# Performance work log

Hardware: AMD Instinct MI355X
Metric: run time of the kernel (lower is better)

## Reference

```python
import jax, jax.numpy as jnp
import numpy as np

D_MODEL = 1024
N_HEADS = 16
HEAD_DIM = D_MODEL // N_HEADS


def setup_inputs() -> dict:
    key = jax.random.key(0)
    k1, k2, k3, k4, k5 = jax.random.split(key, 5)
    s = 1.0 / np.sqrt(D_MODEL)
    return {
        "x": jax.random.normal(k1, (2, 2048, D_MODEL), dtype=jnp.float32),
        "w_qkv": jax.random.normal(k2, (D_MODEL, 3 * D_MODEL), dtype=jnp.float32) * s,
        "b_qkv": jax.random.normal(k3, (3 * D_MODEL,), dtype=jnp.float32) * 0.02,
        "w_proj": jax.random.normal(k4, (D_MODEL, D_MODEL), dtype=jnp.float32) * s,
        "b_proj": jax.random.normal(k5, (D_MODEL,), dtype=jnp.float32) * 0.02,
    }


def reference(x, w_qkv, b_qkv, w_proj, b_proj):
    B, S, D = x.shape
    H, Hd = N_HEADS, HEAD_DIM
    qkv = x @ w_qkv + b_qkv                       # [B,S,3D]
    q, k, v = jnp.split(qkv, 3, axis=-1)
    # split heads -> [B,H,S,Hd]
    q = q.reshape(B, S, H, Hd).transpose(0, 2, 1, 3)
    k = k.reshape(B, S, H, Hd).transpose(0, 2, 1, 3)
    v = v.reshape(B, S, H, Hd).transpose(0, 2, 1, 3)
    scale = 1.0 / jnp.sqrt(jnp.asarray(Hd, dtype=x.dtype))
    scores = jnp.einsum("bhqd,bhkd->bhqk", q, k) * scale  # [B,H,S,S]
    causal = jnp.tril(jnp.ones((S, S), dtype=bool))
    scores = jnp.where(causal, scores, jnp.asarray(-jnp.inf, dtype=scores.dtype))
    attn = jax.nn.softmax(scores, axis=-1)
    out = jnp.einsum("bhqk,bhkd->bhqd", attn, v)  # [B,H,S,Hd]
    out = out.transpose(0, 2, 1, 3).reshape(B, S, D)
    return out @ w_proj + b_proj
```

## Files before the change

kernel.cpp:

```cpp
#include <hip/hip_runtime.h>


typedef float f32x4 __attribute__((ext_vector_type(4)));
typedef float f32x16 __attribute__((ext_vector_type(16)));
typedef short bf16x8 __attribute__((ext_vector_type(8)));

#if __has_builtin(__builtin_amdgcn_exp2f)
#define EXP2(x) __builtin_amdgcn_exp2f(x)
#else
#define EXP2(x) exp2f(x)
#endif

__device__ __forceinline__ unsigned short f2bf(float f) {
  union { float f; unsigned u; } v; v.f = f;
  unsigned u = v.u + 0x7fffu + ((v.u >> 16) & 1u);
  return (unsigned short)(u >> 16);
}

__device__ __forceinline__ void async_load16(const void* g, void* lds) {
  __builtin_amdgcn_global_load_lds(
      (const __attribute__((address_space(1))) void*)g,
      (__attribute__((address_space(3))) void*)lds, 16, 0, 0);
}

__global__ void f32_to_bf16_kernel(const float* __restrict__ in,
                                   unsigned short* __restrict__ out, int n) {
  int i = (blockIdx.x * 256 + threadIdx.x) * 4;
  if (i < n) {
    float4 f = *(const float4*)(in + i);
    ushort4 o;
    o.x = f2bf(f.x); o.y = f2bf(f.y); o.z = f2bf(f.z); o.w = f2bf(f.w);
    *(ushort4*)(out + i) = o;
  }
}

__global__ void transpose_f32_bf16_kernel(const float* __restrict__ in,
                                          unsigned short* __restrict__ out,
                                          int K, int N) {
  __shared__ float tile[32][33];
  int n0 = blockIdx.x * 32, k0 = blockIdx.y * 32;
  int tx = threadIdx.x, ty = threadIdx.y;
#pragma unroll
  for (int i = ty; i < 32; i += 8)
    tile[i][tx] = in[(size_t)(k0 + i) * N + (n0 + tx)];
  __syncthreads();
#pragma unroll
  for (int i = ty; i < 32; i += 8)
    out[(size_t)(n0 + i) * K + (k0 + tx)] = f2bf(tile[tx][i]);
}

template <int MI, int NI>
__device__ __forceinline__ void gemm_mainloop(
    const unsigned short* __restrict__ A,
    const unsigned short* __restrict__ BT,
    int K, int mBlk, int nBlk,
    unsigned short* As, unsigned short* Bs,
    f32x4 (&acc)[MI][NI], int lane, int wave)
{
  const int l16 = lane & 15, quad = lane >> 4;
  const int mW = (wave >> 1) * MI * 16;
  const int nW = (wave & 1) * NI * 16;
  constexpr int AROWS = 2 * MI * 16;
  constexpr int BROWS = 2 * NI * 16;
  constexpr int AINST = AROWS / 64;
  constexpr int BINST = BROWS / 64;
  const int rl = lane >> 2;
  const int cl = (lane & 3) * 8;

  for (int k0 = 0; k0 < K; k0 += 32) {
    __syncthreads();
#pragma unroll
    for (int t = 0; t < AINST; ++t) {
      const int rbase = wave * (AROWS / 4) + t * 16;
      async_load16(A + (size_t)(mBlk + rbase + rl) * K + k0 + cl, &As[rbase * 32]);
    }
#pragma unroll
    for (int t = 0; t < BINST; ++t) {
      const int rbase = wave * (BROWS / 4) + t * 16;
      async_load16(BT + (size_t)(nBlk + rbase + rl) * K + k0 + cl, &Bs[rbase * 32]);
    }
    __syncthreads();

    bf16x8 af[MI], bf[NI];
#pragma unroll
    for (int i = 0; i < MI; ++i)
      af[i] = *(const bf16x8*)&As[(mW + i * 16 + l16) * 32 + quad * 8];
#pragma unroll
    for (int j = 0; j < NI; ++j)
      bf[j] = *(const bf16x8*)&Bs[(nW + j * 16 + l16) * 32 + quad * 8];
#pragma unroll
    for (int i = 0; i < MI; ++i)
#pragma unroll
      for (int j = 0; j < NI; ++j)
        acc[i][j] = __builtin_amdgcn_mfma_f32_16x16x32_bf16(af[i], bf[j], acc[i][j], 0, 0, 0);
  }
}

__global__ __launch_bounds__(512, 2) void qkv_gemm_kernel(
    const unsigned short* __restrict__ A,
    const unsigned short* __restrict__ WT,
    const float* __restrict__ bias,
    unsigned short* __restrict__ QKV)
{
  __shared__ __align__(16) unsigned short Al[2][2][256][32];
  __shared__ __align__(16) unsigned short Bl[2][2][256][32];
  const int lane = threadIdx.x & 63;
  const int wave = threadIdx.x >> 6;
  const int l16 = lane & 15, quad = lane >> 4;
  const int wm = wave >> 2, wn = wave & 3;

  const int bid = blockIdx.x;
  const int swz = (bid & 7) * 24 + (bid >> 3);
  const int bx = swz & 15, by = swz >> 4;
  const int mBlk = bx * 256, nBlk = by * 256;

  const int srow = wave * 32 + (lane >> 2);
  const int scol = lane & 3;

  auto stage = [&](const unsigned short* __restrict__ G, int gRow0,
                   unsigned short (*L)[32], int kOff) {
#pragma unroll
    for (int i = 0; i < 2; ++i) {
      const int row = srow + i * 16;
      const int c = scol ^ ((row >> 1) & 3);
      async_load16(G + (size_t)(gRow0 + row) * 1024 + kOff + c * 8,
                   &L[wave * 32 + i * 16][0]);
    }
  };

  auto rdA = [&](int buf, int kc, int mi) -> bf16x8 {
    const int r = wm * 128 + mi * 16 + l16;
    return *(const bf16x8*)&Al[buf][kc][r][(quad ^ ((r >> 1) & 3)) * 8];
  };
  auto rdB = [&](int buf, int kc, int n) -> bf16x8 {
    const int r = wn * 64 + n * 16 + l16;
    return *(const bf16x8*)&Bl[buf][kc][r][(quad ^ ((r >> 1) & 3)) * 8];
  };

  f32x4 acc[8][4];
  const f32x4 z4 = {0.f, 0.f, 0.f, 0.f};
#pragma unroll
  for (int i = 0; i < 8; ++i)
#pragma unroll
    for (int j = 0; j < 4; ++j) acc[i][j] = z4;

  stage(A, mBlk, Al[0][0], 0);
  stage(WT, nBlk, Bl[0][0], 0);
  stage(A, mBlk, Al[0][1], 32);
  stage(WT, nBlk, Bl[0][1], 32);
  asm volatile("s_waitcnt vmcnt(4)\n\ts_barrier" ::: "memory");

  for (int t = 0; t < 16; ++t) {
    const int cur = t & 1, nxt = cur ^ 1;
    const int tn = (t + 1 < 16) ? t + 1 : 15;
    const int kO = tn * 64;
    bf16x8 bf0[4], bf1[4], af[4];

    stage(A, mBlk, Al[nxt][0], kO);
#pragma unroll
    for (int n = 0; n < 4; ++n) bf0[n] = rdB(cur, 0, n);
#pragma unroll
    for (int mi = 0; mi < 4; ++mi) af[mi] = rdA(cur, 0, mi);
    __builtin_amdgcn_s_setprio(1);
#pragma unroll
    for (int mi = 0; mi < 4; ++mi)
#pragma unroll
      for (int n = 0; n < 4; ++n)
        acc[mi][n] = __builtin_amdgcn_mfma_f32_16x16x32_bf16(af[mi], bf0[n], acc[mi][n], 0, 0, 0);
    __builtin_amdgcn_s_setprio(0);
    asm volatile("s_waitcnt vmcnt(2)\n\ts_barrier" ::: "memory");

    stage(WT, nBlk, Bl[nxt][0], kO);
#pragma unroll
    for (int n = 0; n < 4; ++n) bf1[n] = rdB(cur, 1, n);
#pragma unroll
    for (int mi = 0; mi < 4; ++mi) af[mi] = rdA(cur, 1, mi);
    __builtin_amdgcn_s_setprio(1);
#pragma unroll
    for (int mi = 0; mi < 4; ++mi)
#pragma unroll
      for (int n = 0; n < 4; ++n)
        acc[mi][n] = __builtin_amdgcn_mfma_f32_16x16x32_bf16(af[mi], bf1[n], acc[mi][n], 0, 0, 0);
    __builtin_amdgcn_s_setprio(0);
    asm volatile("s_barrier" ::: "memory");

    stage(A, mBlk, Al[nxt][1], kO + 32);
#pragma unroll
    for (int mi = 0; mi < 4; ++mi) af[mi] = rdA(cur, 0, mi + 4);
    __builtin_amdgcn_s_setprio(1);
#pragma unroll
    for (int mi = 0; mi < 4; ++mi)
#pragma unroll
      for (int n = 0; n < 4; ++n)
        acc[mi + 4][n] = __builtin_amdgcn_mfma_f32_16x16x32_bf16(af[mi], bf0[n], acc[mi + 4][n], 0, 0, 0);
    __builtin_amdgcn_s_setprio(0);
    asm volatile("s_barrier" ::: "memory");

    stage(WT, nBlk, Bl[nxt][1], kO + 32);
#pragma unroll
    for (int mi = 0; mi < 4; ++mi) af[mi] = rdA(cur, 1, mi + 4);
    __builtin_amdgcn_s_setprio(1);
#pragma unroll
    for (int mi = 0; mi < 4; ++mi)
#pragma unroll
      for (int n = 0; n < 4; ++n)
        acc[mi + 4][n] = __builtin_amdgcn_mfma_f32_16x16x32_bf16(af[mi], bf1[n], acc[mi + 4][n], 0, 0, 0);
    __builtin_amdgcn_s_setprio(0);
    asm volatile("s_waitcnt vmcnt(4)\n\ts_barrier" ::: "memory");
  }
  asm volatile("s_waitcnt vmcnt(0)" ::: "memory");

  const int m0 = mBlk + wm * 128;
  const int n0 = nBlk + wn * 64;
  const int whichW = n0 >> 10;
  const int bb = m0 >> 11;
  const int sBase = (m0 & 2047);
  const size_t planeE = (size_t)2 * 16 * 2048 * 64;

  if (whichW == 2) {
    unsigned short* Vb = QKV + 2 * planeE;
#pragma unroll
    for (int j = 0; j < 4; ++j) {
      const int rem = (n0 & 1023) + j * 16 + l16;
      const int hh = rem >> 6, hd = rem & 63;
      const float bv = bias[n0 + j * 16 + l16];
      unsigned short* col = Vb + (((size_t)bb * 16 + hh) * 64 + hd) * 2048;
#pragma unroll
      for (int i = 0; i < 8; ++i) {
        unsigned short pk[4];
#pragma unroll
        for (int r = 0; r < 4; ++r) pk[r] = f2bf(acc[i][j][r] + bv);
        *(ushort4*)&col[sBase + i * 16 + quad * 4] = *(ushort4*)pk;
      }
    }
  } else {
    const float scale = (whichW == 0) ? 0.18033688011112042f : 1.0f;
#pragma unroll
    for (int j = 0; j < 4; ++j) {
      const int n = n0 + j * 16 + l16;
      const float bv = bias[n];
      const int rem = n & 1023;
      const int hh = rem >> 6, hd = rem & 63;
      unsigned short* pl = QKV + (size_t)whichW * planeE +
                           (((size_t)bb * 16 + hh) * 2048) * 64 + hd;
#pragma unroll
      for (int r = 0; r < 4; ++r) {
        const int s = sBase + (quad * 4 + r);
#pragma unroll
        for (int i = 0; i < 8; ++i)
          pl[(size_t)(s + i * 16) * 64] = f2bf((acc[i][j][r] + bv) * scale);
      }
    }
  }
}

__global__ __launch_bounds__(256, 2) void attn_kernel(
    const unsigned short* __restrict__ QKV,
    unsigned short* __restrict__ AO)
{
  __shared__ __align__(16) unsigned short Ks[3 * 64 * 64];
  __shared__ __align__(16) unsigned short Vs[3 * 64 * 64];
  const int lane = threadIdx.x & 63;
  const int wave = threadIdx.x >> 6;
  const int l31 = lane & 31;
  const int hi  = lane >> 5;

  const int lin  = blockIdx.x;
  const int xcd  = lin & 7;
  const int slot = lin >> 3;
  const int col  = xcd * 4 + (slot >> 4);
  const int b = col >> 4, h = col & 15;
  const int qg = (slot < 32) ? (slot & 15) : (15 - (slot & 15));
  const int qw = qg * 128 + wave * 32;

  const size_t planeE = (size_t)2 * 16 * 2048 * 64;
  const size_t bhS = ((size_t)b * 16 + h) * (size_t)(2048 * 64);
  const unsigned short* Q   = QKV + bhS;
  const unsigned short* Kg  = QKV + planeE + bhS;
  const unsigned short* VTg = QKV + 2 * planeE + bhS;

  bf16x8 qf_[4];
#pragma unroll
  for (int t = 0; t < 4; ++t)
    qf_[t] = *(const bf16x8*)(Q + (size_t)(qw + l31) * 64 + t * 16 + hi * 8);

  bf16x8 onesf;
#pragma unroll
  for (int i = 0; i < 8; ++i) onesf[i] = (short)0x3F80;

  f32x16 O[2], Osum;
#pragma unroll
  for (int r = 0; r < 16; ++r) { O[0][r] = 0.f; O[1][r] = 0.f; Osum[r] = 0.f; }

  const int tbase = (wave & 1) * 4;
  const bool doV = wave >= 2;

  auto stage = [&](int tileIdx, int bufIdx) {
    const int kt = tileIdx * 64;
    unsigned short* Kb = Ks + bufIdx * 4096;
    unsigned short* Vb = Vs + bufIdx * 4096;
#pragma unroll
    for (int i = 0; i < 4; ++i) {
      const int t = tbase + i;
      const int s = t * 64 + lane;
      const int row = s >> 3;
      const int c = (s & 7) ^ (row & 7);
      if (doV)
        async_load16(VTg + (size_t)row * 2048 + kt + c * 8, Vb + t * 512);
      else
        async_load16(Kg + (size_t)(kt + row) * 64 + c * 8, Kb + t * 512);
    }
  };

  const int nt = qg * 2 + 2;
  stage(0, 0);
  stage(1, 1);
  for (int ti = 0; ti < nt; ++ti) {
    asm volatile("s_waitcnt vmcnt(4)\n\ts_barrier" ::: "memory");
    const int tn = (ti + 2 < nt) ? ti + 2 : nt - 1;
    stage(tn, (ti + 2) % 3);
    const int kt = ti * 64;
    const unsigned short* Kb = Ks + (ti % 3) * 4096;
    const unsigned short* Vb = Vs + (ti % 3) * 4096;

    if (kt <= qw + 31) {
      const bool dmask = (kt + 63 > qw);
#pragma unroll
      for (int kg = 0; kg < 2; ++kg) {
        const int krow = kg * 32 + l31;
        const int ks7 = krow & 7;
        bf16x8 ka[4];
#pragma unroll
        for (int t = 0; t < 4; ++t)
          ka[t] = *(const bf16x8*)&Kb[(krow * 8 + ((t * 2 + hi) ^ ks7)) * 8];

        f32x16 sc;
#pragma unroll
        for (int r = 0; r < 16; ++r) sc[r] = 0.f;
        __builtin_amdgcn_s_setprio(1);
#pragma unroll
        for (int t = 0; t < 4; ++t)
          sc = __builtin_amdgcn_mfma_f32_32x32x16_bf16(ka[t], qf_[t], sc, 0, 0, 0);
        __builtin_amdgcn_s_setprio(0);

        float p[16];
#pragma unroll
        for (int r = 0; r < 16; ++r) {
          float v = sc[r];
          if (dmask) {
            const int key = kt + kg * 32 + (r & 3) + 8 * (r >> 2) + 4 * hi;
            if (key > qw + l31) v = -INFINITY;
          }
          p[r] = EXP2(v);
        }
        unsigned c8[8];
#pragma unroll
        for (int i = 0; i < 8; ++i)
          asm("v_cvt_pk_bf16_f32 %0, %1, %2"
              : "=v"(c8[i]) : "v"(p[2 * i]), "v"(p[2 * i + 1]));

#pragma unroll
        for (int half = 0; half < 2; ++half) {
          unsigned a0 = c8[4 * half + 0], a1 = c8[4 * half + 1];
          unsigned a2 = c8[4 * half + 2], a3 = c8[4 * half + 3];
          asm("v_permlane32_swap_b32 %0, %1" : "+v"(a0), "+v"(a2));
          asm("v_permlane32_swap_b32 %0, %1" : "+v"(a1), "+v"(a3));
          union { unsigned u[4]; bf16x8 v; } pa;
          pa.u[0] = a0; pa.u[1] = a1; pa.u[2] = a2; pa.u[3] = a3;
          const int kc = kg * 2 + half;

          __builtin_amdgcn_s_setprio(1);
          Osum = __builtin_amdgcn_mfma_f32_32x32x16_bf16(pa.v, onesf, Osum, 0, 0, 0);
#pragma unroll
          for (int g = 0; g < 2; ++g) {
            const int vrow = g * 32 + l31;
            bf16x8 vb = *(const bf16x8*)&Vb[(vrow * 8 + ((kc * 2 + hi) ^ (vrow & 7))) * 8];
            O[g] = __builtin_amdgcn_mfma_f32_32x32x16_bf16(pa.v, vb, O[g], 0, 0, 0);
          }
          __builtin_amdgcn_s_setprio(0);
        }
      }
    }
  }

  unsigned short* base = AO + ((size_t)b * 2048 + qw) * 1024 + h * 64 + l31;
#pragma unroll
  for (int r = 0; r < 16; ++r) {
    const float inv = 1.0f / Osum[r];
    const int row = (r & 3) + 8 * (r >> 2) + 4 * hi;
#pragma unroll
    for (int g = 0; g < 2; ++g)
      base[(size_t)row * 1024 + g * 32] = f2bf(O[g][r] * inv);
  }
}

__global__ __launch_bounds__(256) void proj_gemm_kernel(
    const unsigned short* __restrict__ A,
    const unsigned short* __restrict__ WT,
    const float* __restrict__ bias,
    float* __restrict__ out)
{
  __shared__ unsigned short As[64 * 32];
  __shared__ unsigned short Bs[128 * 32];
  const int lane = threadIdx.x & 63;
  const int wave = threadIdx.x >> 6;
  const int l16 = lane & 15, quad = lane >> 4;

  f32x4 acc[2][4];
  const f32x4 z4 = {0.f, 0.f, 0.f, 0.f};
#pragma unroll
  for (int i = 0; i < 2; ++i)
#pragma unroll
    for (int j = 0; j < 4; ++j) acc[i][j] = z4;

  gemm_mainloop<2, 4>(A, WT, 1024, blockIdx.x * 64, blockIdx.y * 128,
                      As, Bs, acc, lane, wave);

  const int m0 = blockIdx.x * 64 + (wave >> 1) * 32;
  const int n0 = blockIdx.y * 128 + (wave & 1) * 64;
#pragma unroll
  for (int i = 0; i < 2; ++i) {
#pragma unroll
    for (int j = 0; j < 4; ++j) {
      const int n = n0 + j * 16 + l16;
      const float bv = bias[n];
#pragma unroll
      for (int r = 0; r < 4; ++r) {
        const int m = m0 + i * 16 + quad * 4 + r;
        out[(size_t)m * 1024 + n] = acc[i][j][r] + bv;
      }
    }
  }
}

extern "C" void kernel_launch(void* const* d_in, const int* in_sizes, int n_in,
                              void* d_out, int out_size, void* d_ws, size_t ws_size,
                              hipStream_t stream) {
  const float* x      = (const float*)d_in[0];
  const float* w_qkv  = (const float*)d_in[1];
  const float* b_qkv  = (const float*)d_in[2];
  const float* w_proj = (const float*)d_in[3];
  const float* b_proj = (const float*)d_in[4];
  float* out = (float*)d_out;

  unsigned short* Xb  = (unsigned short*)d_ws;
  unsigned short* WTq = Xb + (size_t)4096 * 1024;
  unsigned short* WTp = WTq + (size_t)3072 * 1024;
  unsigned short* QKV = WTp + (size_t)1024 * 1024;
  unsigned short* AO  = QKV + (size_t)3 * 4096 * 1024;

  f32_to_bf16_kernel<<<4096, 256, 0, stream>>>(x, Xb, 4096 * 1024);
  transpose_f32_bf16_kernel<<<dim3(96, 32), dim3(32, 8), 0, stream>>>(w_qkv, WTq, 1024, 3072);
  transpose_f32_bf16_kernel<<<dim3(32, 32), dim3(32, 8), 0, stream>>>(w_proj, WTp, 1024, 1024);
  qkv_gemm_kernel<<<192, 512, 0, stream>>>(Xb, WTq, b_qkv, QKV);
  attn_kernel<<<512, 256, 0, stream>>>(QKV, AO);
  proj_gemm_kernel<<<dim3(64, 8), 256, 0, stream>>>(AO, WTp, b_proj, out);
}
```

Before: 205.0 us.

## Reorder QKV GEMM k-half phases and remap block swizzle per XCD

Changes the block-to-tile mapping so each XCD gets a compact 4x6 tile region rather than a strided set, aiming for better L2 reuse of A and W tiles. Reorders the four MFMA phases to finish k-half 0 for both M halves before k-half 1, which reuses one B fragment set and drops the second bf register array. Adds barriers after LDS reads in each phase and moves the vmcnt wait. The extra barriers may add synchronization stalls in exchange for lower register pressure and tighter sync.

```diff
diff --git a/kernel.cpp b/kernel.cpp
--- a/kernel.cpp
+++ b/kernel.cpp
@@ -110,8 +110,9 @@
   const int wm = wave >> 2, wn = wave & 3;
 
   const int bid = blockIdx.x;
-  const int swz = (bid & 7) * 24 + (bid >> 3);
-  const int bx = swz & 15, by = swz >> 4;
+  const int xcd = bid & 7, rb = bid >> 3;
+  const int bx = (xcd & 3) * 4 + (rb & 3);
+  const int by = (xcd >> 2) * 6 + (rb >> 2);
   const int mBlk = bx * 256, nBlk = by * 256;
 
   const int srow = wave * 32 + (lane >> 2);
@@ -128,13 +129,13 @@
     }
   };
 
-  auto rdA = [&](int buf, int kc, int mi) -> bf16x8 {
+  auto rdA = [&](int buf, int kh, int mi) -> bf16x8 {
     const int r = wm * 128 + mi * 16 + l16;
-    return *(const bf16x8*)&Al[buf][kc][r][(quad ^ ((r >> 1) & 3)) * 8];
+    return *(const bf16x8*)&Al[buf][kh][r][(quad ^ ((r >> 1) & 3)) * 8];
   };
-  auto rdB = [&](int buf, int kc, int n) -> bf16x8 {
+  auto rdB = [&](int buf, int kh, int n) -> bf16x8 {
     const int r = wn * 64 + n * 16 + l16;
-    return *(const bf16x8*)&Bl[buf][kc][r][(quad ^ ((r >> 1) & 3)) * 8];
+    return *(const bf16x8*)&Bl[buf][kh][r][(quad ^ ((r >> 1) & 3)) * 8];
   };
 
   f32x4 acc[8][4];
@@ -154,57 +155,61 @@
     const int cur = t & 1, nxt = cur ^ 1;
     const int tn = (t + 1 < 16) ? t + 1 : 15;
     const int kO = tn * 64;
-    bf16x8 bf0[4], bf1[4], af[4];
+    bf16x8 bf[4], af[4];
 
     stage(A, mBlk, Al[nxt][0], kO);
 #pragma unroll
-    for (int n = 0; n < 4; ++n) bf0[n] = rdB(cur, 0, n);
-#pragma unroll
-    for (int mi = 0; mi < 4; ++mi) af[mi] = rdA(cur, 0, mi);
+    for (int n = 0; n < 4; ++n) bf[n] = rdB(cur, 0, n);
+#pragma unroll
+    for (int i = 0; i < 4; ++i) af[i] = rdA(cur, 0, i);
+    asm volatile("s_barrier" ::: "memory");
     __builtin_amdgcn_s_setprio(1);
 #pragma unroll
-    for (int mi = 0; mi < 4; ++mi)
+    for (int i = 0; i < 4; ++i)
 #pragma unroll
       for (int n = 0; n < 4; ++n)
-        acc[mi][n] = __builtin_amdgcn_mfma_f32_16x16x32_bf16(af[mi], bf0[n], acc[mi][n], 0, 0, 0);
+        acc[i][n] = __builtin_amdgcn_mfma_f32_16x16x32_bf16(af[i], bf[n], acc[i][n], 0, 0, 0);
     __builtin_amdgcn_s_setprio(0);
-    asm volatile("s_waitcnt vmcnt(2)\n\ts_barrier" ::: "memory");
+    asm volatile("s_barrier" ::: "memory");
 
     stage(WT, nBlk, Bl[nxt][0], kO);
 #pragma unroll
-    for (int n = 0; n < 4; ++n) bf1[n] = rdB(cur, 1, n);
-#pragma unroll
-    for (int mi = 0; mi < 4; ++mi) af[mi] = rdA(cur, 1, mi);
+    for (int i = 0; i < 4; ++i) af[i] = rdA(cur, 0, 4 + i);
+    asm volatile("s_barrier" ::: "memory");
     __builtin_amdgcn_s_setprio(1);
 #pragma unroll
-    for (int mi = 0; mi < 4; ++mi)
+    for (int i = 0; i < 4; ++i)
 #pragma unroll
       for (int n = 0; n < 4; ++n)
-        acc[mi][n] = __builtin_amdgcn_mfma_f32_16x16x32_bf16(af[mi], bf1[n], acc[mi][n], 0, 0, 0);
+        acc[4 + i][n] = __builtin_amdgcn_mfma_f32_16x16x32_bf16(af[i], bf[n], acc[4 + i][n], 0, 0, 0);
     __builtin_amdgcn_s_setprio(0);
-    asm volatile("s_barrier" ::: "memory");
+    asm volatile("s_waitcnt vmcnt(4)\n\ts_barrier" ::: "memory");
 
     stage(A, mBlk, Al[nxt][1], kO + 32);
 #pragma unroll
-    for (int mi = 0; mi < 4; ++mi) af[mi] = rdA(cur, 0, mi + 4);
+    for (int n = 0; n < 4; ++n) bf[n] = rdB(cur, 1, n);
+#pragma unroll
+    for (int i = 0; i < 4; ++i) af[i] = rdA(cur, 1, i);
+    asm volatile("s_barrier" ::: "memory");
     __builtin_amdgcn_s_setprio(1);
 #pragma unroll
-    for (int mi = 0; mi < 4; ++mi)
+    for (int i = 0; i < 4; ++i)
 #pragma unroll
       for (int n = 0; n < 4; ++n)
-        acc[mi + 4][n] = __builtin_amdgcn_mfma_f32_16x16x32_bf16(af[mi], bf0[n], acc[mi + 4][n], 0, 0, 0);
+        acc[i][n] = __builtin_amdgcn_mfma_f32_16x16x32_bf16(af[i], bf[n], acc[i][n], 0, 0, 0);
     __builtin_amdgcn_s_setprio(0);
     asm volatile("s_barrier" ::: "memory");
 
     stage(WT, nBlk, Bl[nxt][1], kO + 32);
 #pragma unroll
-    for (int mi = 0; mi < 4; ++mi) af[mi] = rdA(cur, 1, mi + 4);
+    for (int i = 0; i < 4; ++i) af[i] = rdA(cur, 1, 4 + i);
+    asm volatile("s_barrier" ::: "memory");
     __builtin_amdgcn_s_setprio(1);
 #pragma unroll
-    for (int mi = 0; mi < 4; ++mi)
+    for (int i = 0; i < 4; ++i)
 #pragma unroll
       for (int n = 0; n < 4; ++n)
-        acc[mi + 4][n] = __builtin_amdgcn_mfma_f32_16x16x32_bf16(af[mi], bf1[n], acc[mi + 4][n], 0, 0, 0);
+        acc[4 + i][n] = __builtin_amdgcn_mfma_f32_16x16x32_bf16(af[i], bf[n], acc[4 + i][n], 0, 0, 0);
     __builtin_amdgcn_s_setprio(0);
     asm volatile("s_waitcnt vmcnt(4)\n\ts_barrier" ::: "memory");
   }
```

New measurement: 203.3 us. No clear change (-0.8%).
